# Kernel optimization log

Measured on AMD Instinct MI355X. Metric: run time of the kernel, lower is better.

## Reference

```python
import jax, jax.numpy as jnp
import numpy as np

OUTPUT_DIM = 8192
LEAF_DIM = 128
FEAT = 1024
BATCH = 8192
NUM_LEAVES = int(np.ceil(OUTPUT_DIM / LEAF_DIM))          # 64
NUM_INTERNAL = NUM_LEAVES - 1                              # 63
DEPTH = int(np.ceil(np.log2(NUM_LEAVES)))                  # 6


def _build_path_maps():
    # Exactly mirrors the Keras layer's __init__ path-map construction.
    nodes = np.full((NUM_LEAVES, DEPTH), -1, dtype=np.int32)
    dirs_ = np.full((NUM_LEAVES, DEPTH), -1, dtype=np.int32)
    for leaf_idx in range(NUM_LEAVES):
        curr = NUM_INTERNAL + leaf_idx
        path, dirs = [], []
        while curr > 0:
            parent = (curr - 1) // 2
            path.append(parent)
            dirs.append((curr - 1) % 2)
            curr = parent
        n = len(path)
        nodes[leaf_idx, :n] = path[::-1]
        dirs_[leaf_idx, :n] = dirs[::-1]
    return jnp.asarray(nodes), jnp.asarray(dirs_)


def setup_inputs() -> dict:
    key = jax.random.key(0)
    k1, k2, k3 = jax.random.split(key, 3)
    x = jax.random.normal(k1, (BATCH, FEAT), dtype=jnp.float32)
    # glorot-ish scaling for stable softmax / outputs
    routing_weights = jax.random.normal(k2, (NUM_INTERNAL, FEAT, 2), dtype=jnp.float32) * (1.0 / np.sqrt(FEAT))
    leaf_weights = jax.random.normal(k3, (NUM_LEAVES, FEAT, LEAF_DIM), dtype=jnp.float32) * (1.0 / np.sqrt(FEAT))
    leaf_biases = jnp.zeros((NUM_LEAVES, LEAF_DIM), dtype=jnp.float32)
    path_nodes, path_directions = _build_path_maps()
    return {
        "x": x,
        "routing_weights": routing_weights,
        "leaf_weights": leaf_weights,
        "leaf_biases": leaf_biases,
        "path_nodes": path_nodes,
        "path_directions": path_directions,
    }


def reference(x, routing_weights, leaf_weights, leaf_biases, path_nodes, path_directions):
    # 1) Routing probabilities at every internal node: (B, N, 2)
    logits = jnp.einsum("bf,nfd->bnd", x, routing_weights)
    probs = jax.nn.softmax(logits, axis=-1)
    # 2) Path probability per leaf: gather the (node, direction) prob along
    #    each leaf's root-to-leaf path, treating -1 padding as prob 1.
    safe_nodes = jnp.maximum(path_nodes, 0)        # (L, D)
    safe_dirs = jnp.maximum(path_directions, 0)    # (L, D)
    step_probs = probs[:, safe_nodes, safe_dirs]   # (B, L, D)
    step_probs = jnp.where(path_nodes[None, :, :] >= 0, step_probs, 1.0)
    leaf_probs = jnp.prod(step_probs, axis=-1)     # (B, L)
    # 3) Batched per-leaf dense: (B, L, d)
    leaf_outputs = jnp.einsum("bf,lfo->blo", x, leaf_weights) + leaf_biases[None, :, :]
    # 4) Weight and concat ('concat' combination, linear activation)
    weighted = leaf_probs[:, :, None] * leaf_outputs
    return weighted.reshape(x.shape[0], -1)        # (B, L*d)
```

## Files before the change

### kernel.cpp

```cpp
#include <hip/hip_runtime.h>


typedef __attribute__((ext_vector_type(8))) short short8;
typedef __attribute__((ext_vector_type(4))) float f32x4;

#define BATCH 8192
#define FEAT  1024
#define NLEAF 64
#define LEAFD 128
#define OUTD  8192

__device__ __forceinline__ unsigned short f2bf(float f) {
    union { float f; unsigned int u; } c; c.f = f;
    unsigned int u = c.u;
    return (unsigned short)((u + 0x7FFFu + ((u >> 16) & 1u)) >> 16);
}

__device__ __forceinline__ void gload16(const void* g, void* l) {
    __builtin_amdgcn_global_load_lds(
        (const __attribute__((address_space(1))) unsigned int*)g,
        (__attribute__((address_space(3))) unsigned int*)l, 16, 0, 0);
}


__global__ __launch_bounds__(256) void cvt_x(const float* __restrict__ x,
                                             unsigned short* __restrict__ xb) {
    const int i = (blockIdx.x * 256 + threadIdx.x) * 4;
    const float4 v = *(const float4*)(x + i);
    ushort4 o;
    o.x = f2bf(v.x); o.y = f2bf(v.y); o.z = f2bf(v.z); o.w = f2bf(v.w);
    *(ushort4*)(xb + i) = o;
}

__global__ __launch_bounds__(256) void cvt_lw(const float* __restrict__ lw,
                                              unsigned short* __restrict__ wt) {
    __shared__ float tile[32][33];
    const int l  = blockIdx.x;
    const int k0 = blockIdx.y * 32;
    const int o0 = blockIdx.z * 32;
    const int tr = threadIdx.x >> 5;
    const int tc = threadIdx.x & 31;
    const float* src = lw + (size_t)l * (FEAT * LEAFD);
#pragma unroll
    for (int p = 0; p < 4; ++p) {
        const int r = p * 8 + tr;
        tile[r][tc] = src[(size_t)(k0 + r) * LEAFD + o0 + tc];
    }
    __syncthreads();
    unsigned short* dst = wt + (size_t)l * (LEAFD * FEAT);
#pragma unroll
    for (int p = 0; p < 4; ++p) {
        const int oo = p * 8 + tr;
        dst[(size_t)(o0 + oo) * FEAT + k0 + tc] = f2bf(tile[tc][oo]);
    }
}

__global__ __launch_bounds__(256) void cvt_rw(const float* __restrict__ rw,
                                              unsigned short* __restrict__ rt) {
    const int gid = blockIdx.x * 256 + threadIdx.x;
    const int row = gid >> 10;
    const int f   = gid & 1023;
    const float v = (row < 126) ? rw[(size_t)(row >> 1) * 2048 + f * 2 + (row & 1)] : 0.0f;
    rt[gid] = f2bf(v);
}

__global__ __launch_bounds__(256) void routing_gemm(
        const unsigned short* __restrict__ xb,
        const unsigned short* __restrict__ rt,
        float* __restrict__ logits) {
    __shared__ __align__(16) unsigned short As[128 * 32];
    __shared__ __align__(16) unsigned short Bs[128 * 32];
    const int t    = threadIdx.x;
    const int row0 = blockIdx.x * 128;
    const int wv = t >> 6, ln = t & 63;
    const int wm = wv >> 1, wn = wv & 1;
    const int quad = ln >> 4, r16 = ln & 15;

    f32x4 acc[4][4];
#pragma unroll
    for (int i = 0; i < 4; ++i)
#pragma unroll
        for (int j = 0; j < 4; ++j) acc[i][j] = (f32x4)0.0f;

    const unsigned short* ag = xb + (size_t)row0 * FEAT;
    const int srow = t >> 2;
    const int scol = (t & 3) * 8;

    for (int k0 = 0; k0 < FEAT; k0 += 32) {
#pragma unroll
        for (int i = 0; i < 2; ++i) {
            gload16(ag + (size_t)(i * 64 + srow) * FEAT + k0 + scol,
                    (char*)As + i * 4096 + t * 16);
            gload16(rt + (size_t)(i * 64 + srow) * FEAT + k0 + scol,
                    (char*)Bs + i * 4096 + t * 16);
        }
        __syncthreads();
        short8 a[4], b[4];
#pragma unroll
        for (int mi = 0; mi < 4; ++mi)
            a[mi] = *(const short8*)&As[(wm * 64 + mi * 16 + r16) * 32 + quad * 8];
#pragma unroll
        for (int ni = 0; ni < 4; ++ni)
            b[ni] = *(const short8*)&Bs[(wn * 64 + ni * 16 + r16) * 32 + quad * 8];
#pragma unroll
        for (int mi = 0; mi < 4; ++mi)
#pragma unroll
            for (int ni = 0; ni < 4; ++ni)
                acc[mi][ni] = __builtin_amdgcn_mfma_f32_16x16x32_bf16(
                    a[mi], b[ni], acc[mi][ni], 0, 0, 0);
        __syncthreads();
    }
#pragma unroll
    for (int mi = 0; mi < 4; ++mi) {
        const int r = wm * 64 + mi * 16 + quad * 4;
#pragma unroll
        for (int ni = 0; ni < 4; ++ni) {
            const int c = wn * 64 + ni * 16 + r16;
#pragma unroll
            for (int reg = 0; reg < 4; ++reg)
                logits[(size_t)(row0 + r + reg) * 128 + c] = acc[mi][ni][reg];
        }
    }
}

__global__ __launch_bounds__(256) void leafprob(
        const float* __restrict__ logits,
        const int* __restrict__ pnodes,
        const int* __restrict__ pdirs,
        float* __restrict__ lp) {
    const int gid  = blockIdx.x * 256 + threadIdx.x;
    const int b    = gid >> 6;
    const int leaf = gid & 63;
    float prod = 1.0f;
#pragma unroll
    for (int d = 0; d < 6; ++d) {
        const int n   = pnodes[leaf * 6 + d];
        const int dir = pdirs[leaf * 6 + d];
        if (n >= 0) {
            const float z0 = logits[(size_t)b * 128 + n * 2];
            const float z1 = logits[(size_t)b * 128 + n * 2 + 1];
            const float zd = dir ? z1 : z0;
            const float zo = dir ? z0 : z1;
            prod *= 1.0f / (1.0f + __expf(zo - zd));
        }
    }
    lp[gid] = prod;
}

__global__ __launch_bounds__(256) void leaf_gemm(
        const unsigned short* __restrict__ xb,
        const unsigned short* __restrict__ wt,
        const float* __restrict__ lp,
        const float* __restrict__ bias,
        float* __restrict__ out) {
    __shared__ __align__(16) unsigned short As[128 * 32];
    __shared__ __align__(16) unsigned short Bs[128 * 32];
    __shared__ float lps[128];
    __shared__ float bs[128];

    const int t    = threadIdx.x;
    const int row0 = blockIdx.x * 128;
    const int l    = blockIdx.y;

    if (t < 128) {
        lps[t] = lp[(size_t)(row0 + t) * NLEAF + l];
        bs[t]  = bias[l * LEAFD + t];
    }

    const int wv = t >> 6, ln = t & 63;
    const int wm = wv >> 1, wn = wv & 1;
    const int quad = ln >> 4, r16 = ln & 15;

    f32x4 acc[4][4];
#pragma unroll
    for (int i = 0; i < 4; ++i)
#pragma unroll
        for (int j = 0; j < 4; ++j) acc[i][j] = (f32x4)0.0f;

    const unsigned short* ag = xb + (size_t)row0 * FEAT;
    const unsigned short* bg = wt + (size_t)l * (LEAFD * FEAT);
    const int srow = t >> 2;
    const int scol = (t & 3) * 8;

    for (int k0 = 0; k0 < FEAT; k0 += 32) {
#pragma unroll
        for (int i = 0; i < 2; ++i) {
            gload16(ag + (size_t)(i * 64 + srow) * FEAT + k0 + scol,
                    (char*)As + i * 4096 + t * 16);
            gload16(bg + (size_t)(i * 64 + srow) * FEAT + k0 + scol,
                    (char*)Bs + i * 4096 + t * 16);
        }
        __syncthreads();
        short8 a[4], b[4];
#pragma unroll
        for (int mi = 0; mi < 4; ++mi)
            a[mi] = *(const short8*)&As[(wm * 64 + mi * 16 + r16) * 32 + quad * 8];
#pragma unroll
        for (int ni = 0; ni < 4; ++ni)
            b[ni] = *(const short8*)&Bs[(wn * 64 + ni * 16 + r16) * 32 + quad * 8];
#pragma unroll
        for (int mi = 0; mi < 4; ++mi)
#pragma unroll
            for (int ni = 0; ni < 4; ++ni)
                acc[mi][ni] = __builtin_amdgcn_mfma_f32_16x16x32_bf16(
                    a[mi], b[ni], acc[mi][ni], 0, 0, 0);
        __syncthreads();
    }

#pragma unroll
    for (int mi = 0; mi < 4; ++mi) {
        const int r = wm * 64 + mi * 16 + quad * 4;
#pragma unroll
        for (int ni = 0; ni < 4; ++ni) {
            const int c  = wn * 64 + ni * 16 + r16;
            const float bv = bs[c];
#pragma unroll
            for (int reg = 0; reg < 4; ++reg) {
                const float v = (acc[mi][ni][reg] + bv) * lps[r + reg];
                out[(size_t)(row0 + r + reg) * OUTD + l * LEAFD + c] = v;
            }
        }
    }
}


extern "C" void kernel_launch(void* const* d_in, const int* in_sizes, int n_in,
                              void* d_out, int out_size, void* d_ws, size_t ws_size,
                              hipStream_t stream) {
    const float* x    = (const float*)d_in[0];
    const float* rw   = (const float*)d_in[1];
    const float* lw   = (const float*)d_in[2];
    const float* bias = (const float*)d_in[3];
    const int*   pn   = (const int*)d_in[4];
    const int*   pd   = (const int*)d_in[5];
    float* out = (float*)d_out;

    char* ws = (char*)d_ws;
    unsigned short* xb     = (unsigned short*)(ws);
    unsigned short* wt     = (unsigned short*)(ws + 16777216);
    unsigned short* rt     = (unsigned short*)(ws + 33554432);
    float*          logits = (float*)(ws + 33816576);
    float*          lpv    = (float*)(ws + 38010880);

    cvt_x<<<8192, 256, 0, stream>>>(x, xb);
    cvt_lw<<<dim3(64, 32, 4), 256, 0, stream>>>(lw, wt);
    cvt_rw<<<512, 256, 0, stream>>>(rw, rt);
    routing_gemm<<<64, 256, 0, stream>>>(xb, rt, logits);
    leafprob<<<2048, 256, 0, stream>>>(logits, pn, pd, lpv);
    leaf_gemm<<<dim3(64, 64), 256, 0, stream>>>(xb, wt, lpv, bias, out);
}
```

Measured before the change: 507.4 us.

## Fuse leaf-prob into leaf GEMM, use 32x32 MFMA, swizzle LDS, vectorize weight transpose

Removes the separate leafprob kernel and computes each block's path probabilities inside leaf_gemm from the routing logits. Both GEMMs switch from 16x16x32 to 32x32x16 bf16 MFMA with an XOR-swizzled LDS layout to avoid bank conflicts. The K loop reads fragments into registers before issuing the next tile's global-to-LDS load, so the load overlaps the MFMAs. The weight transpose kernel now uses float4 loads and 16-byte stores. The price is redundant path-probability work per leaf block, 64-wide strided logits reads in the GEMM prologue, and epilogue stores that touch more rows per register group.

```diff
diff --git a/kernel.cpp b/kernel.cpp
--- a/kernel.cpp
+++ b/kernel.cpp
@@ -1,8 +1,9 @@
 #include <hip/hip_runtime.h>
 
 
-typedef __attribute__((ext_vector_type(8))) short short8;
-typedef __attribute__((ext_vector_type(4))) float f32x4;
+typedef __attribute__((ext_vector_type(8)))  short short8;
+typedef __attribute__((ext_vector_type(4)))  float f32x4;
+typedef __attribute__((ext_vector_type(16))) float f32x16;
 
 #define BATCH 8192
 #define FEAT  1024
@@ -34,25 +35,31 @@
 
 __global__ __launch_bounds__(256) void cvt_lw(const float* __restrict__ lw,
                                               unsigned short* __restrict__ wt) {
-    __shared__ float tile[32][33];
+    __shared__ float tile[64][33];
     const int l  = blockIdx.x;
-    const int k0 = blockIdx.y * 32;
+    const int k0 = blockIdx.y * 64;
     const int o0 = blockIdx.z * 32;
-    const int tr = threadIdx.x >> 5;
-    const int tc = threadIdx.x & 31;
-    const float* src = lw + (size_t)l * (FEAT * LEAFD);
-#pragma unroll
-    for (int p = 0; p < 4; ++p) {
-        const int r = p * 8 + tr;
-        tile[r][tc] = src[(size_t)(k0 + r) * LEAFD + o0 + tc];
+    const int t  = threadIdx.x;
+    const float* src = lw + (size_t)l * (FEAT * LEAFD) + (size_t)k0 * LEAFD + o0;
+    {
+        const int fc = (t & 7) * 4;
+        const int r  = t >> 3;
+#pragma unroll
+        for (int p = 0; p < 2; ++p) {
+            const float4 v = *(const float4*)(src + (size_t)(r + p * 32) * LEAFD + fc);
+            tile[r + p * 32][fc]     = v.x;
+            tile[r + p * 32][fc + 1] = v.y;
+            tile[r + p * 32][fc + 2] = v.z;
+            tile[r + p * 32][fc + 3] = v.w;
+        }
     }
     __syncthreads();
-    unsigned short* dst = wt + (size_t)l * (LEAFD * FEAT);
-#pragma unroll
-    for (int p = 0; p < 4; ++p) {
-        const int oo = p * 8 + tr;
-        dst[(size_t)(o0 + oo) * FEAT + k0 + tc] = f2bf(tile[tc][oo]);
-    }
+    const int o  = t >> 3;
+    const int kg = (t & 7) * 8;
+    short8 u;
+#pragma unroll
+    for (int j = 0; j < 8; ++j) u[j] = (short)f2bf(tile[kg + j][o]);
+    *(short8*)(wt + (size_t)l * (LEAFD * FEAT) + (size_t)(o0 + o) * FEAT + k0 + kg) = u;
 }
 
 __global__ __launch_bounds__(256) void cvt_rw(const float* __restrict__ rw,
@@ -62,6 +69,27 @@
     const int f   = gid & 1023;
     const float v = (row < 126) ? rw[(size_t)(row >> 1) * 2048 + f * 2 + (row & 1)] : 0.0f;
     rt[gid] = f2bf(v);
+}
+
+
+__device__ __forceinline__ void stage_tile(const unsigned short* __restrict__ ag,
+                                           const unsigned short* __restrict__ bg,
+                                           int k0, int t,
+                                           unsigned short* As, unsigned short* Bs) {
+    const int srow = t >> 2;
+    const int scol = ((t & 3) ^ (srow & 3)) * 8;
+#pragma unroll
+    for (int i = 0; i < 2; ++i) {
+        gload16(ag + (size_t)(i * 64 + srow) * FEAT + k0 + scol,
+                (char*)As + i * 4096 + t * 16);
+        gload16(bg + (size_t)(i * 64 + srow) * FEAT + k0 + scol,
+                (char*)Bs + i * 4096 + t * 16);
+    }
+}
+
+__device__ __forceinline__ short8 frag(const unsigned short* S, int row, int kstep, int half) {
+    const int p = ((kstep * 2 + half) ^ (row & 3));
+    return *(const short8*)&S[row * 32 + p * 8];
 }
 
 __global__ __launch_bounds__(256) void routing_gemm(
@@ -74,84 +102,61 @@
     const int row0 = blockIdx.x * 128;
     const int wv = t >> 6, ln = t & 63;
     const int wm = wv >> 1, wn = wv & 1;
-    const int quad = ln >> 4, r16 = ln & 15;
-
-    f32x4 acc[4][4];
-#pragma unroll
-    for (int i = 0; i < 4; ++i)
-#pragma unroll
-        for (int j = 0; j < 4; ++j) acc[i][j] = (f32x4)0.0f;
+    const int c32 = ln & 31, half = ln >> 5;
+
+    f32x16 acc[2][2];
+#pragma unroll
+    for (int i = 0; i < 2; ++i)
+#pragma unroll
+        for (int j = 0; j < 2; ++j) acc[i][j] = (f32x16)0.0f;
 
     const unsigned short* ag = xb + (size_t)row0 * FEAT;
-    const int srow = t >> 2;
-    const int scol = (t & 3) * 8;
-
-    for (int k0 = 0; k0 < FEAT; k0 += 32) {
-#pragma unroll
-        for (int i = 0; i < 2; ++i) {
-            gload16(ag + (size_t)(i * 64 + srow) * FEAT + k0 + scol,
-                    (char*)As + i * 4096 + t * 16);
-            gload16(rt + (size_t)(i * 64 + srow) * FEAT + k0 + scol,
-                    (char*)Bs + i * 4096 + t * 16);
-        }
-        __syncthreads();
-        short8 a[4], b[4];
-#pragma unroll
-        for (int mi = 0; mi < 4; ++mi)
-            a[mi] = *(const short8*)&As[(wm * 64 + mi * 16 + r16) * 32 + quad * 8];
-#pragma unroll
-        for (int ni = 0; ni < 4; ++ni)
-            b[ni] = *(const short8*)&Bs[(wn * 64 + ni * 16 + r16) * 32 + quad * 8];
-#pragma unroll
-        for (int mi = 0; mi < 4; ++mi)
-#pragma unroll
-            for (int ni = 0; ni < 4; ++ni)
-                acc[mi][ni] = __builtin_amdgcn_mfma_f32_16x16x32_bf16(
-                    a[mi], b[ni], acc[mi][ni], 0, 0, 0);
-        __syncthreads();
-    }
-#pragma unroll
-    for (int mi = 0; mi < 4; ++mi) {
-        const int r = wm * 64 + mi * 16 + quad * 4;
-#pragma unroll
-        for (int ni = 0; ni < 4; ++ni) {
-            const int c = wn * 64 + ni * 16 + r16;
-#pragma unroll
-            for (int reg = 0; reg < 4; ++reg)
-                logits[(size_t)(row0 + r + reg) * 128 + c] = acc[mi][ni][reg];
-        }
-    }
-}
-
-__global__ __launch_bounds__(256) void leafprob(
-        const float* __restrict__ logits,
-        const int* __restrict__ pnodes,
-        const int* __restrict__ pdirs,
-        float* __restrict__ lp) {
-    const int gid  = blockIdx.x * 256 + threadIdx.x;
-    const int b    = gid >> 6;
-    const int leaf = gid & 63;
-    float prod = 1.0f;
-#pragma unroll
-    for (int d = 0; d < 6; ++d) {
-        const int n   = pnodes[leaf * 6 + d];
-        const int dir = pdirs[leaf * 6 + d];
-        if (n >= 0) {
-            const float z0 = logits[(size_t)b * 128 + n * 2];
-            const float z1 = logits[(size_t)b * 128 + n * 2 + 1];
-            const float zd = dir ? z1 : z0;
-            const float zo = dir ? z0 : z1;
-            prod *= 1.0f / (1.0f + __expf(zo - zd));
-        }
-    }
-    lp[gid] = prod;
+
+    stage_tile(ag, rt, 0, t, As, Bs);
+    for (int kk = 0; kk < FEAT / 32; ++kk) {
+        __syncthreads();
+        short8 a[2][2], b[2][2];
+#pragma unroll
+        for (int mi = 0; mi < 2; ++mi)
+#pragma unroll
+            for (int ks = 0; ks < 2; ++ks)
+                a[mi][ks] = frag(As, wm * 64 + mi * 32 + c32, ks, half);
+#pragma unroll
+        for (int ni = 0; ni < 2; ++ni)
+#pragma unroll
+            for (int ks = 0; ks < 2; ++ks)
+                b[ni][ks] = frag(Bs, wn * 64 + ni * 32 + c32, ks, half);
+        __syncthreads();
+        if (kk + 1 < FEAT / 32) stage_tile(ag, rt, (kk + 1) * 32, t, As, Bs);
+#pragma unroll
+        for (int mi = 0; mi < 2; ++mi)
+#pragma unroll
+            for (int ni = 0; ni < 2; ++ni)
+#pragma unroll
+                for (int ks = 0; ks < 2; ++ks)
+                    acc[mi][ni] = __builtin_amdgcn_mfma_f32_32x32x16_bf16(
+                        a[mi][ks], b[ni][ks], acc[mi][ni], 0, 0, 0);
+    }
+#pragma unroll
+    for (int mi = 0; mi < 2; ++mi)
+#pragma unroll
+        for (int ni = 0; ni < 2; ++ni) {
+            const int c = wn * 64 + ni * 32 + c32;
+#pragma unroll
+            for (int reg = 0; reg < 16; ++reg) {
+                const int r = wm * 64 + mi * 32 + (reg & 3) + 8 * (reg >> 2) + 4 * half;
+                logits[(size_t)(row0 + r) * 128 + c] = acc[mi][ni][reg];
+            }
+        }
 }
 
 __global__ __launch_bounds__(256) void leaf_gemm(
         const unsigned short* __restrict__ xb,
         const unsigned short* __restrict__ wt,
-        const float* __restrict__ lp,
+        const float* __restrict__ logits,
         const float* __restrict__ bias,
+        const int* __restrict__ pn,
+        const int* __restrict__ pd,
         float* __restrict__ out) {
     __shared__ __align__(16) unsigned short As[128 * 32];
     __shared__ __align__(16) unsigned short Bs[128 * 32];
@@ -162,65 +167,77 @@
     const int row0 = blockIdx.x * 128;
     const int l    = blockIdx.y;
 
+    const unsigned short* ag = xb + (size_t)row0 * FEAT;
+    const unsigned short* bg = wt + (size_t)l * (LEAFD * FEAT);
+
+    stage_tile(ag, bg, 0, t, As, Bs);
+
     if (t < 128) {
-        lps[t] = lp[(size_t)(row0 + t) * NLEAF + l];
-        bs[t]  = bias[l * LEAFD + t];
+        bs[t] = bias[l * LEAFD + t];
+        const int b = row0 + t;
+        float prod = 1.0f;
+#pragma unroll
+        for (int d = 0; d < 6; ++d) {
+            const int n   = pn[l * 6 + d];
+            const int dir = pd[l * 6 + d];
+            if (n >= 0) {
+                const float z0 = logits[(size_t)b * 128 + n * 2];
+                const float z1 = logits[(size_t)b * 128 + n * 2 + 1];
+                const float delta = dir ? (z1 - z0) : (z0 - z1);
+                prod *= 1.0f / (1.0f + __expf(-delta));
+            }
+        }
+        lps[t] = prod;
     }
 
     const int wv = t >> 6, ln = t & 63;
     const int wm = wv >> 1, wn = wv & 1;
-    const int quad = ln >> 4, r16 = ln & 15;
-
-    f32x4 acc[4][4];
-#pragma unroll
-    for (int i = 0; i < 4; ++i)
-#pragma unroll
-        for (int j = 0; j < 4; ++j) acc[i][j] = (f32x4)0.0f;
-
-    const unsigned short* ag = xb + (size_t)row0 * FEAT;
-    const unsigned short* bg = wt + (size_t)l * (LEAFD * FEAT);
-    const int srow = t >> 2;
-    const int scol = (t & 3) * 8;
-
-    for (int k0 = 0; k0 < FEAT; k0 += 32) {
-#pragma unroll
-        for (int i = 0; i < 2; ++i) {
-            gload16(ag + (size_t)(i * 64 + srow) * FEAT + k0 + scol,
-                    (char*)As + i * 4096 + t * 16);
-            gload16(bg + (size_t)(i * 64 + srow) * FEAT + k0 + scol,
-                    (char*)Bs + i * 4096 + t * 16);
-        }
-        __syncthreads();
-        short8 a[4], b[4];
-#pragma unroll
-        for (int mi = 0; mi < 4; ++mi)
-            a[mi] = *(const short8*)&As[(wm * 64 + mi * 16 + r16) * 32 + quad * 8];
-#pragma unroll
-        for (int ni = 0; ni < 4; ++ni)
-            b[ni] = *(const short8*)&Bs[(wn * 64 + ni * 16 + r16) * 32 + quad * 8];
-#pragma unroll
-        for (int mi = 0; mi < 4; ++mi)
-#pragma unroll
-            for (int ni = 0; ni < 4; ++ni)
-                acc[mi][ni] = __builtin_amdgcn_mfma_f32_16x16x32_bf16(
-                    a[mi], b[ni], acc[mi][ni], 0, 0, 0);
-        __syncthreads();
-    }
-
-#pragma unroll
-    for (int mi = 0; mi < 4; ++mi) {
-        const int r = wm * 64 + mi * 16 + quad * 4;
-#pragma unroll
-        for (int ni = 0; ni < 4; ++ni) {
-            const int c  = wn * 64 + ni * 16 + r16;
+    const int c32 = ln & 31, half = ln >> 5;
+
+    f32x16 acc[2][2];
+#pragma unroll
+    for (int i = 0; i < 2; ++i)
+#pragma unroll
+        for (int j = 0; j < 2; ++j) acc[i][j] = (f32x16)0.0f;
+
+    for (int kk = 0; kk < FEAT / 32; ++kk) {
+        __syncthreads();
+        short8 a[2][2], b[2][2];
+#pragma unroll
+        for (int mi = 0; mi < 2; ++mi)
+#pragma unroll
+            for (int ks = 0; ks < 2; ++ks)
+                a[mi][ks] = frag(As, wm * 64 + mi * 32 + c32, ks, half);
+#pragma unroll
+        for (int ni = 0; ni < 2; ++ni)
+#pragma unroll
+            for (int ks = 0; ks < 2; ++ks)
+                b[ni][ks] = frag(Bs, wn * 64 + ni * 32 + c32, ks, half);
+        __syncthreads();
+        if (kk + 1 < FEAT / 32) stage_tile(ag, bg, (kk + 1) * 32, t, As, Bs);
+#pragma unroll
+        for (int mi = 0; mi < 2; ++mi)
+#pragma unroll
+            for (int ni = 0; ni < 2; ++ni)
+#pragma unroll
+                for (int ks = 0; ks < 2; ++ks)
+                    acc[mi][ni] = __builtin_amdgcn_mfma_f32_32x32x16_bf16(
+                        a[mi][ks], b[ni][ks], acc[mi][ni], 0, 0, 0);
+    }
+
+#pragma unroll
+    for (int mi = 0; mi < 2; ++mi)
+#pragma unroll
+        for (int ni = 0; ni < 2; ++ni) {
+            const int c  = wn * 64 + ni * 32 + c32;
             const float bv = bs[c];
 #pragma unroll
-            for (int reg = 0; reg < 4; ++reg) {
-                const float v = (acc[mi][ni][reg] + bv) * lps[r + reg];
-                out[(size_t)(row0 + r + reg) * OUTD + l * LEAFD + c] = v;
+            for (int reg = 0; reg < 16; ++reg) {
+                const int r = wm * 64 + mi * 32 + (reg & 3) + 8 * (reg >> 2) + 4 * half;
+                const float v = (acc[mi][ni][reg] + bv) * lps[r];
+                out[(size_t)(row0 + r) * OUTD + l * LEAFD + c] = v;
             }
         }
-    }
 }
 
 
@@ -240,12 +257,10 @@
     unsigned short* wt     = (unsigned short*)(ws + 16777216);
     unsigned short* rt     = (unsigned short*)(ws + 33554432);
     float*          logits = (float*)(ws + 33816576);
-    float*          lpv    = (float*)(ws + 38010880);
 
     cvt_x<<<8192, 256, 0, stream>>>(x, xb);
-    cvt_lw<<<dim3(64, 32, 4), 256, 0, stream>>>(lw, wt);
+    cvt_lw<<<dim3(64, 16, 4), 256, 0, stream>>>(lw, wt);
     cvt_rw<<<512, 256, 0, stream>>>(rw, rt);
     routing_gemm<<<64, 256, 0, stream>>>(xb, rt, logits);
-    leafprob<<<2048, 256, 0, stream>>>(logits, pn, pd, lpv);
-    leaf_gemm<<<dim3(64, 64), 256, 0, stream>>>(xb, wt, lpv, bias, out);
-}
+    leaf_gemm<<<dim3(64, 64), 256, 0, stream>>>(xb, wt, logits, bias, pn, pd, out);
+}
```

Result: slower. 522.6 us (+3.0%).
